# Performance work log

Measured on AMD Instinct MI355X. Metric: run time of the kernel, lower is better.

The kernel has to match this reference:

```python
import jax, jax.numpy as jnp
import numpy as np

NUM_HEADS = 16


def setup_inputs() -> dict:
    key = jax.random.key(0)
    ks = jax.random.split(key, 5)
    S, B, N, C = 4, 2, 2048, 1024
    return {
        "x_all": jax.random.normal(ks[0], (S, B, N, C), dtype=jnp.float32),
        "w_qkv": jax.random.normal(ks[1], (C, 3 * C), dtype=jnp.float32) * (C ** -0.5),
        "b_qkv": jax.random.normal(ks[2], (3 * C,), dtype=jnp.float32) * 0.02,
        "w_proj": jax.random.normal(ks[3], (C, C), dtype=jnp.float32) * (C ** -0.5),
        "b_proj": jax.random.normal(ks[4], (C,), dtype=jnp.float32) * 0.02,
    }


def reference(x_all, w_qkv, b_qkv, w_proj, b_proj):
    # x_all: [S, B, N, C] -- S = cp_dim ring shards, each rank holds [B, N, C]
    S, B, N, C = x_all.shape
    H = NUM_HEADS
    D = C // H
    scale = 1.0 / np.sqrt(D).astype(np.float32)

    # same qkv projection on every rank
    qkv = (jnp.einsum("sbnc,ce->sbne", x_all, w_qkv) + b_qkv)
    qkv = qkv.reshape(S, B, N, 3, H, D)
    # rank 0's queries: [B, H, N, D]
    q = jnp.transpose(qkv[0, :, :, 0], (0, 2, 1, 3))
    # all shards' keys/values: [S, B, H, N, D]
    k = jnp.transpose(qkv[:, :, :, 1], (0, 1, 3, 2, 4))
    v = jnp.transpose(qkv[:, :, :, 2], (0, 1, 3, 2, 4))

    # ring loop: online softmax merge across KV shards (numerically stable
    # form of the source's exp(lse)-weighted average)
    attn_out, lse = None, None
    for s in range(S):
        scores = jnp.einsum("bhnd,bhmd->bhnm", q, k[s]) * scale  # [B,H,N,N]
        new_lse = jax.nn.logsumexp(scores, axis=-1)               # [B,H,N]
        probs = jnp.exp(scores - new_lse[..., None])
        new_out = jnp.einsum("bhnm,bhmd->bhnd", probs, v[s])      # [B,H,N,D]
        if attn_out is None:
            attn_out, lse = new_out, new_lse
        else:
            m = jnp.logaddexp(lse, new_lse)
            attn_out = (attn_out * jnp.exp(lse - m)[..., None]
                        + new_out * jnp.exp(new_lse - m)[..., None])
            lse = m

    # [B,H,N,D] -> [B,N,C]
    out = jnp.transpose(attn_out, (0, 2, 1, 3)).reshape(B, N, C)
    return out @ w_proj + b_proj
```

## Files before the change

kernel.cpp:

```cpp
#include <hip/hip_runtime.h>
#include <hip/hip_bf16.h>


typedef __bf16 bf16x8 __attribute__((ext_vector_type(8)));
typedef float v4f __attribute__((ext_vector_type(4)));

#if __has_builtin(__builtin_amdgcn_exp2f)
#define EXP2F(x) __builtin_amdgcn_exp2f(x)
#else
#define EXP2F(x) exp2f(x)
#endif

__device__ __forceinline__ float bf2f(unsigned short h) {
  union { unsigned int u; float f; } a; a.u = ((unsigned int)h) << 16; return a.f;
}
__device__ __forceinline__ unsigned short f2bf(float f) {
  union { float f; unsigned int u; } a; a.f = f;
  unsigned int u = a.u;
  unsigned int r = (u + 0x7fffu + ((u >> 16) & 1u)) >> 16;
  return (unsigned short)r;
}
__device__ __forceinline__ unsigned int pack2t(float a, float b) {
  union { float f; unsigned int u; } ua, ub; ua.f = a; ub.f = b;
#if __has_builtin(__builtin_amdgcn_perm)
  return __builtin_amdgcn_perm(ub.u, ua.u, 0x07060302u);
#else
  return (ua.u >> 16) | (ub.u & 0xffff0000u);
#endif
}
__device__ __forceinline__ bf16x8 ldfrag16(const unsigned short* p) {
  union { uint4 u; bf16x8 v; } x; x.u = *(const uint4*)p; return x.v;
}
__device__ __forceinline__ bf16x8 ones8() {
  union { unsigned short s[8]; bf16x8 v; } x;
#pragma unroll
  for (int i = 0; i < 8; i++) x.s[i] = 0x3F80;
  return x.v;
}
__device__ __forceinline__ void gld_lds16(const unsigned short* g, unsigned short* l) {
  __builtin_amdgcn_global_load_lds((__attribute__((address_space(1))) void*)g,
                                   (__attribute__((address_space(3))) void*)l, 16, 0, 0);
}

__global__ void detect_dtype(const unsigned short* __restrict__ x, int* flag) {
  __shared__ int cnt;
  if (threadIdx.x == 0) cnt = 0;
  __syncthreads();
  int sane = 0;
#pragma unroll
  for (int j = 0; j < 4; j++) {
    unsigned short v = x[2 * (threadIdx.x + 64 * j)];
    int e = (v >> 7) & 0xFF;
    if (e >= 90 && e <= 140) sane++;
  }
  atomicAdd(&cnt, sane);
  __syncthreads();
  if (threadIdx.x == 0) *flag = (cnt > 160) ? 0 : 1;
}

__global__ void conv_to_bf16(const void* __restrict__ in, unsigned short* __restrict__ out,
                             int n4, const int* __restrict__ flag) {
  int i = blockIdx.x * blockDim.x + threadIdx.x;
  if (i >= n4) return;
  if (*flag) {
    float4 v = ((const float4*)in)[i];
    ushort4 o;
    o.x = f2bf(v.x); o.y = f2bf(v.y); o.z = f2bf(v.z); o.w = f2bf(v.w);
    ((ushort4*)out)[i] = o;
  } else {
    ((ushort4*)out)[i] = ((const ushort4*)in)[i];
  }
}

__global__ void conv_bias(const void* __restrict__ bq_in, const void* __restrict__ bp_in,
                          unsigned short* __restrict__ bq, unsigned short* __restrict__ bp,
                          const int* __restrict__ flag) {
  int i = blockIdx.x * 256 + threadIdx.x;
  const void* in = (i < 768) ? bq_in : bp_in;
  unsigned short* out = (i < 768) ? bq : bp;
  int j = (i < 768) ? i : i - 768;
  if (*flag) {
    float4 v = ((const float4*)in)[j];
    ushort4 o;
    o.x = f2bf(v.x); o.y = f2bf(v.y); o.z = f2bf(v.z); o.w = f2bf(v.w);
    ((ushort4*)out)[j] = o;
  } else {
    ((ushort4*)out)[j] = ((const ushort4*)in)[j];
  }
}

__global__ void trans_both(const void* __restrict__ wqkv, const void* __restrict__ wproj,
                           unsigned short* __restrict__ wt1, unsigned short* __restrict__ wt2,
                           const int* __restrict__ flag) {
  __shared__ unsigned short t[32][33];
  int tx = threadIdx.x, ty = threadIdx.y;
  int bx = blockIdx.x;
  const void* in; unsigned short* out; int C, c0;
  if (bx < 96) { in = wqkv; out = wt1; C = 3072; c0 = bx * 32; }
  else         { in = wproj; out = wt2; C = 1024; c0 = (bx - 96) * 32; }
  const int R = 1024;
  int r0 = blockIdx.y * 32;
  int fp = *flag;
#pragma unroll
  for (int j = 0; j < 32; j += 8) {
    unsigned short v;
    if (fp) v = f2bf(((const float*)in)[(r0 + ty + j) * C + c0 + tx]);
    else    v = ((const unsigned short*)in)[(r0 + ty + j) * C + c0 + tx];
    t[ty + j][tx] = v;
  }
  __syncthreads();
#pragma unroll
  for (int j = 0; j < 32; j += 8) out[(c0 + ty + j) * R + r0 + tx] = t[tx][ty + j];
}

template <int MODE>
__launch_bounds__(256, 3)
__global__ void gemm_bt(const unsigned short* __restrict__ A,
                        const unsigned short* __restrict__ Bt,
                        const unsigned short* __restrict__ bias,
                        void* __restrict__ Cout,
                        int K, int ldc, const int* __restrict__ flag,
                        const unsigned short* Bt2, const unsigned short* bias2,
                        void* Cout2,
                        const unsigned short* Bt3, const unsigned short* bias3,
                        void* Cout3) {
  __shared__ unsigned short As[128 * 32];
  __shared__ unsigned short Bs[128 * 32];
  int tid = threadIdx.x;
  int w = tid >> 6, lane = tid & 63, col = lane & 15, quad = lane >> 4;
  int wm = w >> 1, wn = w & 1;
  const unsigned short* Bt_ = Bt;
  const unsigned short* bias_ = bias;
  void* Cout_ = Cout;
  bool isq = false, isv = false;
  int n0, m0;
  if constexpr (MODE == 4) {
    int id = blockIdx.x;
    int xcd = id & 7, t = id >> 3;
    n0 = (t & 7) * 128;
    int y = xcd * 36 + (t >> 3);
    if (y < 256) {
      m0 = (y >> 1) * 128;
      if (y & 1) { isv = true; Bt_ = Bt3; bias_ = bias3; Cout_ = Cout3; }
    } else {
      m0 = (y - 256) * 128;
      isq = true; Bt_ = Bt2; bias_ = bias2; Cout_ = Cout2;
    }
  } else {
    int id = blockIdx.x;
    int xcd = id & 7, t = id >> 3;
    n0 = (t & 7) * 128;
    m0 = (xcd * 4 + (t >> 3)) * 128;
  }
  int fp = 0;
  if constexpr (MODE == 2) fp = *flag;

  v4f acc[4][4];
#pragma unroll
  for (int i = 0; i < 4; i++)
#pragma unroll
    for (int j = 0; j < 4; j++) acc[i][j] = v4f{0.f, 0.f, 0.f, 0.f};

  int ra0 = tid >> 2, cc = tid & 3;
  const unsigned short* ga0 = &A[(m0 + ra0) * K + cc * 8];
  const unsigned short* ga1 = ga0 + 64 * K;
  const unsigned short* gb0 = &Bt_[(n0 + ra0) * K + cc * 8];
  const unsigned short* gb1 = gb0 + 64 * K;
  unsigned short* lA0 = &As[(w * 16) * 32];
  unsigned short* lA1 = &As[(64 + w * 16) * 32];
  unsigned short* lB0 = &Bs[(w * 16) * 32];
  unsigned short* lB1 = &Bs[(64 + w * 16) * 32];

  int niter = K >> 5;
  for (int it = 0; it < niter; it++) {
    __syncthreads();
    gld_lds16(ga0, lA0); gld_lds16(ga1, lA1);
    gld_lds16(gb0, lB0); gld_lds16(gb1, lB1);
    ga0 += 32; ga1 += 32; gb0 += 32; gb1 += 32;
    __syncthreads();
    bf16x8 af[4], bfr[4];
#pragma unroll
    for (int mi = 0; mi < 4; mi++) af[mi] = ldfrag16(&As[(wm * 64 + mi * 16 + col) * 32 + quad * 8]);
#pragma unroll
    for (int ni = 0; ni < 4; ni++) bfr[ni] = ldfrag16(&Bs[(wn * 64 + ni * 16 + col) * 32 + quad * 8]);
#pragma unroll
    for (int mi = 0; mi < 4; mi++)
#pragma unroll
      for (int ni = 0; ni < 4; ni++)
        acc[mi][ni] = __builtin_amdgcn_mfma_f32_16x16x32_bf16(af[mi], bfr[ni], acc[mi][ni], 0, 0, 0);
  }

  float bv[4];
#pragma unroll
  for (int ni = 0; ni < 4; ni++) bv[ni] = bf2f(bias_[n0 + wn * 64 + ni * 16 + col]);

  if (MODE == 4 && isv) {
    int rgb0 = m0 + wm * 64;
    int s = rgb0 >> 12, b = (rgb0 >> 11) & 1, n = rgb0 & 2047;
    int kvg0 = s * 2048 + n;
#pragma unroll
    for (int ni = 0; ni < 4; ni++) {
      int cg = n0 + wn * 64 + ni * 16 + col;
      int h = cg >> 6, d = cg & 63;
      unsigned short* rowp = &((unsigned short*)Cout_)[((b * 16 + h) * 64 + d) * 8192 + kvg0];
      float bvn = bv[ni];
#pragma unroll
      for (int r = 0; r < 4; r++) {
        ushort2 e, o2;
        e.x = f2bf(acc[0][ni][r] + bvn);
        e.y = f2bf(acc[2][ni][r] + bvn);
        o2.x = f2bf(acc[1][ni][r] + bvn);
        o2.y = f2bf(acc[3][ni][r] + bvn);
        *(ushort2*)&rowp[2 * (quad * 4 + r)] = e;
        *(ushort2*)&rowp[32 + 2 * (quad * 4 + r)] = o2;
      }
    }
  } else {
#pragma unroll
    for (int mi = 0; mi < 4; mi++)
#pragma unroll
      for (int ni = 0; ni < 4; ni++) {
        float vals[4];
#pragma unroll
        for (int r = 0; r < 4; r++) vals[r] = acc[mi][ni][r] + bv[ni];
        if constexpr (MODE == 4) {
          if (isq) {
#pragma unroll
            for (int r = 0; r < 4; r++) vals[r] *= 0.1803368801111601f;
          }
        }
        int rgb = m0 + wm * 64 + mi * 16 + quad * 4;
        int cg  = n0 + wn * 64 + ni * 16 + col;
        if constexpr (MODE == 4) {
          unsigned short* C = (unsigned short*)Cout_;
#pragma unroll
          for (int r = 0; r < 4; r++) C[(rgb + r) * ldc + cg] = f2bf(vals[r]);
        } else {
          if (fp) {
            float* C = (float*)Cout_;
#pragma unroll
            for (int r = 0; r < 4; r++) C[(rgb + r) * ldc + cg] = vals[r];
          } else {
            unsigned short* C = (unsigned short*)Cout_;
#pragma unroll
            for (int r = 0; r < 4; r++) C[(rgb + r) * ldc + cg] = f2bf(vals[r]);
          }
        }
      }
  }
}

__launch_bounds__(512, 4)
__global__ void attn_kernel(const unsigned short* __restrict__ qbuf,
                            const unsigned short* __restrict__ kbuf,
                            const unsigned short* __restrict__ vt,
                            float* __restrict__ po,
                            float* __restrict__ lbuf) {
  __shared__ unsigned short Ks[2][64 * 64];
  __shared__ unsigned short Vs[3][64 * 64];
  int tid = threadIdx.x;
  int w = tid >> 6, lane = tid & 63, col = lane & 15, quad = lane >> 4;
  int id = blockIdx.x;
  int xcd = id & 7, slot = id >> 3;
  int qt = slot & 7, gsub = slot >> 3;
  int g = gsub * 8 + xcd;
  int bh = g >> 1, half = g & 1;
  int b = bh >> 4, h = bh & 15;
  int q0 = qt * 256;

  bf16x8 aQ[2][2];
#pragma unroll
  for (int mj = 0; mj < 2; mj++)
#pragma unroll
    for (int kk = 0; kk < 2; kk++)
      aQ[mj][kk] = ldfrag16(&qbuf[(b * 2048 + q0 + w * 32 + mj * 16 + col) * 1024 +
                                  h * 64 + kk * 32 + quad * 8]);

  int r0 = tid >> 3, c0 = tid & 7;
  const unsigned short* kp = &kbuf[((half * 2) * 4096 + b * 2048 + r0) * 1024 + h * 64 + c0 * 8];
  const unsigned short* vp = &vt[(bh * 64 + r0) * 8192 + half * 4096 + c0 * 8];
  int sdst = r0 * 64 + 8 * (c0 ^ (r0 & 7));

  const bf16x8 vone = ones8();
  v4f o[2][4];
  v4f acc_l[2] = {v4f{0.f, 0.f, 0.f, 0.f}, v4f{0.f, 0.f, 0.f, 0.f}};
#pragma unroll
  for (int mj = 0; mj < 2; mj++)
#pragma unroll
    for (int di = 0; di < 4; di++) o[mj][di] = v4f{0.f, 0.f, 0.f, 0.f};

  {
    uint4 k0 = *(const uint4*)kp, v0 = *(const uint4*)vp;
    *(uint4*)&Ks[0][sdst] = k0;
    *(uint4*)&Vs[0][sdst] = v0;
  }
  kp += 64 * 1024; vp += 64;
  uint4 pk = *(const uint4*)kp, pv = *(const uint4*)vp;
  __syncthreads();

  bf16x8 aP[2][2];
  {
    v4f sc[4][2];
#pragma unroll
    for (int ni = 0; ni < 4; ni++)
#pragma unroll
      for (int mj = 0; mj < 2; mj++) sc[ni][mj] = v4f{0.f, 0.f, 0.f, 0.f};
#pragma unroll
    for (int kk = 0; kk < 2; kk++) {
      bf16x8 aK[4];
#pragma unroll
      for (int ni = 0; ni < 4; ni++) {
        int row = ni * 16 + col;
        aK[ni] = ldfrag16(&Ks[0][row * 64 + 8 * ((kk * 4 + quad) ^ (col & 7))]);
      }
#pragma unroll
      for (int ni = 0; ni < 4; ni++)
#pragma unroll
        for (int mj = 0; mj < 2; mj++)
          sc[ni][mj] = __builtin_amdgcn_mfma_f32_16x16x32_bf16(aK[ni], aQ[mj][kk], sc[ni][mj], 0, 0, 0);
    }
#pragma unroll
    for (int ni = 0; ni < 4; ni++)
#pragma unroll
      for (int mj = 0; mj < 2; mj++)
#pragma unroll
        for (int r = 0; r < 4; r++) sc[ni][mj][r] = EXP2F(sc[ni][mj][r]);
#pragma unroll
    for (int mj = 0; mj < 2; mj++)
#pragma unroll
      for (int kk = 0; kk < 2; kk++) {
        union { unsigned int d[4]; bf16x8 v; } u;
#pragma unroll
        for (int t = 0; t < 4; t++)
          u.d[t] = pack2t(sc[kk][mj][t], sc[kk + 2][mj][t]);
        aP[mj][kk] = u.v;
      }
  }
  *(uint4*)&Ks[1][sdst] = pk;
  *(uint4*)&Vs[1][sdst] = pv;
  __syncthreads();

  const unsigned short* vprev = Vs[0];
  const unsigned short* vcur  = Vs[1];
  const unsigned short* vnext = Vs[2];

  for (int t = 1; t < 64; t++) {
    const unsigned short* kcur = Ks[t & 1];
    unsigned short* knxt = (unsigned short*)Ks[(t + 1) & 1];
    if (t < 63) {
      int kstep = (((t + 1) & 31) == 0) ? (2048 + 64) * 1024 : 64 * 1024;
      kp += kstep; vp += 64;
      pk = *(const uint4*)kp; pv = *(const uint4*)vp;
    }

    v4f sc[4][2];
#pragma unroll
    for (int ni = 0; ni < 4; ni++)
#pragma unroll
      for (int mj = 0; mj < 2; mj++) sc[ni][mj] = v4f{0.f, 0.f, 0.f, 0.f};
#pragma unroll
    for (int kk = 0; kk < 2; kk++) {
      bf16x8 aK[4];
#pragma unroll
      for (int ni = 0; ni < 4; ni++) {
        int row = ni * 16 + col;
        aK[ni] = ldfrag16(&kcur[row * 64 + 8 * ((kk * 4 + quad) ^ (col & 7))]);
      }
#pragma unroll
      for (int ni = 0; ni < 4; ni++)
#pragma unroll
        for (int mj = 0; mj < 2; mj++)
          sc[ni][mj] = __builtin_amdgcn_mfma_f32_16x16x32_bf16(aK[ni], aQ[mj][kk], sc[ni][mj], 0, 0, 0);
    }

#pragma unroll
    for (int kk = 0; kk < 2; kk++) {
#pragma unroll
      for (int mj = 0; mj < 2; mj++)
        acc_l[mj] = __builtin_amdgcn_mfma_f32_16x16x32_bf16(aP[mj][kk], vone, acc_l[mj], 0, 0, 0);
      bf16x8 bV[4];
#pragma unroll
      for (int di = 0; di < 4; di++) {
        int row = di * 16 + col;
        bV[di] = ldfrag16(&vprev[row * 64 + 8 * ((kk * 4 + quad) ^ (col & 7))]);
      }
#pragma unroll
      for (int mj = 0; mj < 2; mj++)
#pragma unroll
        for (int di = 0; di < 4; di++)
          o[mj][di] = __builtin_amdgcn_mfma_f32_16x16x32_bf16(aP[mj][kk], bV[di], o[mj][di], 0, 0, 0);
    }

#pragma unroll
    for (int ni = 0; ni < 4; ni++)
#pragma unroll
      for (int mj = 0; mj < 2; mj++)
#pragma unroll
        for (int r = 0; r < 4; r++) sc[ni][mj][r] = EXP2F(sc[ni][mj][r]);
    bf16x8 aPn[2][2];
#pragma unroll
    for (int mj = 0; mj < 2; mj++)
#pragma unroll
      for (int kk = 0; kk < 2; kk++) {
        union { unsigned int d[4]; bf16x8 v; } u;
#pragma unroll
        for (int tt = 0; tt < 4; tt++)
          u.d[tt] = pack2t(sc[kk][mj][tt], sc[kk + 2][mj][tt]);
        aPn[mj][kk] = u.v;
      }

    if (t < 63) {
      *(uint4*)&knxt[sdst] = pk;
      *(uint4*)&((unsigned short*)vnext)[sdst] = pv;
    }

    __syncthreads();

#pragma unroll
    for (int mj = 0; mj < 2; mj++)
#pragma unroll
      for (int kk = 0; kk < 2; kk++) aP[mj][kk] = aPn[mj][kk];
    const unsigned short* vt_ = vprev;
    vprev = vcur; vcur = vnext; vnext = vt_;
  }

#pragma unroll
  for (int kk = 0; kk < 2; kk++) {
#pragma unroll
    for (int mj = 0; mj < 2; mj++)
      acc_l[mj] = __builtin_amdgcn_mfma_f32_16x16x32_bf16(aP[mj][kk], vone, acc_l[mj], 0, 0, 0);
    bf16x8 bV[4];
#pragma unroll
    for (int di = 0; di < 4; di++) {
      int row = di * 16 + col;
      bV[di] = ldfrag16(&vprev[row * 64 + 8 * ((kk * 4 + quad) ^ (col & 7))]);
    }
#pragma unroll
    for (int mj = 0; mj < 2; mj++)
#pragma unroll
      for (int di = 0; di < 4; di++)
        o[mj][di] = __builtin_amdgcn_mfma_f32_16x16x32_bf16(aP[mj][kk], bV[di], o[mj][di], 0, 0, 0);
  }

  float* pb = po + half * 4194304;
#pragma unroll
  for (int mj = 0; mj < 2; mj++)
#pragma unroll
    for (int r = 0; r < 4; r++) {
      int n = q0 + w * 32 + mj * 16 + quad * 4 + r;
      if (col == 0) lbuf[half * 65536 + (b * 16 + h) * 2048 + n] = acc_l[mj][r];
#pragma unroll
      for (int di = 0; di < 4; di++) {
        int c = h * 64 + di * 16 + col;
        pb[(b * 2048 + n) * 1024 + c] = o[mj][di][r];
      }
    }
}

__global__ void merge_halves(const float* __restrict__ po, const float* __restrict__ lbuf,
                             unsigned short* __restrict__ attn) {
  int i = blockIdx.x * 256 + threadIdx.x;
  int r = i >> 8, c4 = i & 255;
  float l = lbuf[((r >> 11) * 16 + (c4 >> 4)) * 2048 + (r & 2047)] +
            lbuf[65536 + ((r >> 11) * 16 + (c4 >> 4)) * 2048 + (r & 2047)];
  float inv = 1.f / l;
  float4 a = ((const float4*)po)[i];
  float4 b = ((const float4*)po)[1048576 + i];
  ushort4 o;
  o.x = f2bf((a.x + b.x) * inv); o.y = f2bf((a.y + b.y) * inv);
  o.z = f2bf((a.z + b.z) * inv); o.w = f2bf((a.w + b.w) * inv);
  ((ushort4*)attn)[i] = o;
}

extern "C" void kernel_launch(void* const* d_in, const int* in_sizes, int n_in,
                              void* d_out, int out_size, void* d_ws, size_t ws_size,
                              hipStream_t stream) {
  const void* x      = d_in[0];
  const void* w_qkv  = d_in[1];
  const void* b_qkv  = d_in[2];
  const void* w_proj = d_in[3];
  const void* b_proj = d_in[4];

  char* ws = (char*)d_ws;
  unsigned short* xb   = (unsigned short*)(ws);
  unsigned short* kk   = (unsigned short*)(ws + 33554432);
  unsigned short* vt   = (unsigned short*)(ws + 67108864);
  unsigned short* q0b  = (unsigned short*)(ws + 100663296);
  unsigned short* attn = (unsigned short*)(ws + 109051904);
  unsigned short* wt1  = (unsigned short*)(ws + 117440512);
  unsigned short* wt2  = (unsigned short*)(ws + 123731968);
  unsigned short* bq   = (unsigned short*)(ws + 125829120);
  unsigned short* bp   = (unsigned short*)(ws + 125835264);
  int* flag            = (int*)(ws + 125837312);
  float* po   = (float*)xb;
  float* lbuf = (float*)wt1;

  detect_dtype<<<1, 64, 0, stream>>>((const unsigned short*)x, flag);

  conv_to_bf16<<<16384, 256, 0, stream>>>(x, xb, 4194304, flag);
  conv_bias<<<4, 256, 0, stream>>>(b_qkv, b_proj, bq, bp, flag);
  trans_both<<<dim3(128, 32), dim3(32, 8), 0, stream>>>(w_qkv, w_proj, wt1, wt2, flag);

  gemm_bt<4><<<2304, 256, 0, stream>>>(xb, wt1 + 1024 * 1024, bq + 1024, kk,
                                       1024, 1024, flag,
                                       wt1, bq, q0b,
                                       wt1 + 2048 * 1024, bq + 2048, vt);

  attn_kernel<<<512, 512, 0, stream>>>(q0b, kk, vt, po, lbuf);
  merge_halves<<<4096, 256, 0, stream>>>(po, lbuf, attn);

  gemm_bt<2><<<256, 256, 0, stream>>>(attn, wt2, bp, d_out,
                                      1024, 1024, flag,
                                      nullptr, nullptr, nullptr,
                                      nullptr, nullptr, nullptr);
}
```

Measured before the change: 287.3 us.

## Double GEMM K-tile to 64 with XOR-swizzled LDS layout

The GEMM main loop now stages a 128x64 K-slab of A and B per iteration instead of 128x32. This halves the number of barrier pairs and loop iterations, and doubles MFMA work per sync. The global-to-LDS load addresses are XOR-swizzled by row so that fragment reads from the wider rows avoid LDS bank conflicts. LDS use per block doubles to 32 KB, which may pressure occupancy under the 3-blocks-per-SM launch bound.

```diff
diff --git a/kernel.cpp b/kernel.cpp
--- a/kernel.cpp
+++ b/kernel.cpp
@@ -124,8 +124,8 @@
                         void* Cout2,
                         const unsigned short* Bt3, const unsigned short* bias3,
                         void* Cout3) {
-  __shared__ unsigned short As[128 * 32];
-  __shared__ unsigned short Bs[128 * 32];
+  __shared__ unsigned short As[128 * 64];
+  __shared__ unsigned short Bs[128 * 64];
   int tid = threadIdx.x;
   int w = tid >> 6, lane = tid & 63, col = lane & 15, quad = lane >> 4;
   int wm = w >> 1, wn = w & 1;
@@ -161,33 +161,55 @@
 #pragma unroll
     for (int j = 0; j < 4; j++) acc[i][j] = v4f{0.f, 0.f, 0.f, 0.f};
 
-  int ra0 = tid >> 2, cc = tid & 3;
-  const unsigned short* ga0 = &A[(m0 + ra0) * K + cc * 8];
-  const unsigned short* ga1 = ga0 + 64 * K;
-  const unsigned short* gb0 = &Bt_[(n0 + ra0) * K + cc * 8];
-  const unsigned short* gb1 = gb0 + 64 * K;
-  unsigned short* lA0 = &As[(w * 16) * 32];
-  unsigned short* lA1 = &As[(64 + w * 16) * 32];
-  unsigned short* lB0 = &Bs[(w * 16) * 32];
-  unsigned short* lB1 = &Bs[(64 + w * 16) * 32];
-
-  int niter = K >> 5;
+  int row0 = tid >> 3, c0 = tid & 7;
+  int sw = c0;
+  int cg0 = (sw ^ (row0 & 7)) * 8;
+  const unsigned short* ga0 = &A[(m0 + row0) * K + cg0];
+  const unsigned short* ga1 = ga0 + 32 * K;
+  const unsigned short* ga2 = ga0 + 64 * K;
+  const unsigned short* ga3 = ga0 + 96 * K;
+  const unsigned short* gb0 = &Bt_[(n0 + row0) * K + cg0];
+  const unsigned short* gb1 = gb0 + 32 * K;
+  const unsigned short* gb2 = gb0 + 64 * K;
+  const unsigned short* gb3 = gb0 + 96 * K;
+  unsigned short* lA0 = &As[w * 512];
+  unsigned short* lA1 = &As[2048 + w * 512];
+  unsigned short* lA2 = &As[4096 + w * 512];
+  unsigned short* lA3 = &As[6144 + w * 512];
+  unsigned short* lB0 = &Bs[w * 512];
+  unsigned short* lB1 = &Bs[2048 + w * 512];
+  unsigned short* lB2 = &Bs[4096 + w * 512];
+  unsigned short* lB3 = &Bs[6144 + w * 512];
+
+  int niter = K >> 6;
   for (int it = 0; it < niter; it++) {
     __syncthreads();
     gld_lds16(ga0, lA0); gld_lds16(ga1, lA1);
+    gld_lds16(ga2, lA2); gld_lds16(ga3, lA3);
     gld_lds16(gb0, lB0); gld_lds16(gb1, lB1);
-    ga0 += 32; ga1 += 32; gb0 += 32; gb1 += 32;
+    gld_lds16(gb2, lB2); gld_lds16(gb3, lB3);
+    ga0 += 64; ga1 += 64; ga2 += 64; ga3 += 64;
+    gb0 += 64; gb1 += 64; gb2 += 64; gb3 += 64;
     __syncthreads();
-    bf16x8 af[4], bfr[4];
-#pragma unroll
-    for (int mi = 0; mi < 4; mi++) af[mi] = ldfrag16(&As[(wm * 64 + mi * 16 + col) * 32 + quad * 8]);
-#pragma unroll
-    for (int ni = 0; ni < 4; ni++) bfr[ni] = ldfrag16(&Bs[(wn * 64 + ni * 16 + col) * 32 + quad * 8]);
-#pragma unroll
-    for (int mi = 0; mi < 4; mi++)
-#pragma unroll
-      for (int ni = 0; ni < 4; ni++)
-        acc[mi][ni] = __builtin_amdgcn_mfma_f32_16x16x32_bf16(af[mi], bfr[ni], acc[mi][ni], 0, 0, 0);
+#pragma unroll
+    for (int kk = 0; kk < 2; kk++) {
+      bf16x8 af[4], bfr[4];
+#pragma unroll
+      for (int mi = 0; mi < 4; mi++) {
+        int row = wm * 64 + mi * 16 + col;
+        af[mi] = ldfrag16(&As[row * 64 + 8 * ((kk * 4 + quad) ^ (col & 7))]);
+      }
+#pragma unroll
+      for (int ni = 0; ni < 4; ni++) {
+        int row = wn * 64 + ni * 16 + col;
+        bfr[ni] = ldfrag16(&Bs[row * 64 + 8 * ((kk * 4 + quad) ^ (col & 7))]);
+      }
+#pragma unroll
+      for (int mi = 0; mi < 4; mi++)
+#pragma unroll
+        for (int ni = 0; ni < 4; ni++)
+          acc[mi][ni] = __builtin_amdgcn_mfma_f32_16x16x32_bf16(af[mi], bfr[ni], acc[mi][ni], 0, 0, 0);
+    }
   }
 
   float bv[4];
```

Result: faster. 265.4 us (-7.6%).
